# Kernel tuning notes

Measured on AMD Instinct MI355X. Metric: run time of the kernel, lower is better.

The kernel has to match this reference:

```python
import jax, jax.numpy as jnp
import numpy as np

N_USERS, N_ITEMS, N_ARTISTS, N_ALBUMS = 100000, 500000, 100000, 200000
D = 128
B, K = 4096, 64


def setup_inputs() -> dict:
    key = jax.random.key(0)
    ks = jax.random.split(key, 12)
    std = 1.0 / np.sqrt(D)
    pairs_u = jax.random.randint(ks[0], (B, 1), 0, N_USERS)
    pairs_i = jax.random.randint(ks[1], (B, 1), 0, N_ITEMS)
    return {
        "user_positive_items_pairs": jnp.concatenate([pairs_u, pairs_i], axis=1),
        "pos_artists": jax.random.randint(ks[2], (B,), 0, N_ARTISTS),
        "pos_albums": jax.random.randint(ks[3], (B,), 0, N_ALBUMS),
        "neg_samples": jax.random.randint(ks[4], (B, K), 0, N_ITEMS),
        "neg_artists": jax.random.randint(ks[5], (B, K), 0, N_ARTISTS),
        "neg_albums": jax.random.randint(ks[6], (B, K), 0, N_ALBUMS),
        "titles": jax.random.randint(ks[7], (B, 1), 0, 50000),
        "titles_len": jnp.ones((B,), dtype=jnp.int32),
        "Wu": jax.random.normal(ks[8], (N_USERS, D), dtype=jnp.float32) * std,
        "Wi": jax.random.normal(ks[9], (N_ITEMS, D), dtype=jnp.float32) * std,
        "Wart": jax.random.normal(ks[10], (N_ARTISTS, D), dtype=jnp.float32) * std,
        "Walb": jax.random.normal(ks[11], (N_ALBUMS, D), dtype=jnp.float32) * std,
    }


def reference(user_positive_items_pairs, pos_artists, pos_albums, neg_samples,
              neg_artists, neg_albums, titles, titles_len, Wu, Wi, Wart, Walb):
    # users: (B, D)
    users = Wu[user_positive_items_pairs[:, 0]]
    # positive combined item embedding: (B, D)
    pos_items = (Wi[user_positive_items_pairs[:, 1]] + Wart[pos_artists] + Walb[pos_albums]) / 3.0
    pos_distances = jnp.sum((users - pos_items) ** 2, axis=1)  # (B,)
    # negative combined item embeddings: (B, K, D)
    neg_items = (Wi[neg_samples] + Wart[neg_artists] + Walb[neg_albums]) / 3.0
    # squared distance to each negative: (B, K)
    distance_to_neg_items = jnp.sum((users[:, None, :] - neg_items) ** 2, axis=2)
    closest_negative_item_distances = jnp.min(distance_to_neg_items, axis=1)  # (B,)
    return pos_distances, distance_to_neg_items, closest_negative_item_distances
```

## Files before the change

kernel.cpp:

```cpp
#include <hip/hip_runtime.h>
#include <math.h>


__device__ __forceinline__ float halfwave_sum(float v) {
    #pragma unroll
    for (int off = 16; off; off >>= 1) v += __shfl_xor(v, off);
    return v;
}

__global__ __launch_bounds__(256) void cml_dist_kernel(
    const int* __restrict__ pairs,
    const int* __restrict__ pos_art,
    const int* __restrict__ pos_alb,
    const int* __restrict__ neg_samp,
    const int* __restrict__ neg_art,
    const int* __restrict__ neg_alb,
    const float4* __restrict__ Wu,
    const float4* __restrict__ Wi,
    const float4* __restrict__ Wart,
    const float4* __restrict__ Walb,
    float* __restrict__ out_pos,
    float* __restrict__ out_dist,
    float* __restrict__ out_min,
    int Kn)
{
    const int b    = blockIdx.x;
    const int tid  = threadIdx.x;
    const int lane = tid & 31;
    const int hw   = tid >> 5;

    __shared__ float s_dist[64];

    const int u_idx = pairs[2 * b];
    const float4 u = Wu[(size_t)u_idx * 32 + lane];

    const float inv3 = 1.0f / 3.0f;

    if (hw == 0) {
        const int ii = pairs[2 * b + 1];
        const int ia = pos_art[b];
        const int il = pos_alb[b];
        const float4 a = Wi  [(size_t)ii * 32 + lane];
        const float4 r = Wart[(size_t)ia * 32 + lane];
        const float4 l = Walb[(size_t)il * 32 + lane];
        const float dx = u.x - (a.x + r.x + l.x) * inv3;
        const float dy = u.y - (a.y + r.y + l.y) * inv3;
        const float dz = u.z - (a.z + r.z + l.z) * inv3;
        const float dw = u.w - (a.w + r.w + l.w) * inv3;
        float acc = dx * dx + dy * dy + dz * dz + dw * dw;
        acc = halfwave_sum(acc);
        if (lane == 0) out_pos[b] = acc;
    }

    for (int kk = hw; kk < Kn; kk += 8) {
        const int base = b * Kn + kk;
        const int ii = neg_samp[base];
        const int ia = neg_art [base];
        const int il = neg_alb [base];
        const float4 a = Wi  [(size_t)ii * 32 + lane];
        const float4 r = Wart[(size_t)ia * 32 + lane];
        const float4 l = Walb[(size_t)il * 32 + lane];
        const float dx = u.x - (a.x + r.x + l.x) * inv3;
        const float dy = u.y - (a.y + r.y + l.y) * inv3;
        const float dz = u.z - (a.z + r.z + l.z) * inv3;
        const float dw = u.w - (a.w + r.w + l.w) * inv3;
        float acc = dx * dx + dy * dy + dz * dz + dw * dw;
        acc = halfwave_sum(acc);
        if (lane == 0) {
            out_dist[base] = acc;
            s_dist[kk]     = acc;
        }
    }

    __syncthreads();

    if (tid < 64) {
        float v = (tid < Kn) ? s_dist[tid] : INFINITY;
        #pragma unroll
        for (int off = 32; off; off >>= 1) {
            const float o = __shfl_down(v, off, 64);
            v = fminf(v, o);
        }
        if (tid == 0) out_min[b] = v;
    }
}

extern "C" void kernel_launch(void* const* d_in, const int* in_sizes, int n_in,
                              void* d_out, int out_size, void* d_ws, size_t ws_size,
                              hipStream_t stream) {
    const int* pairs    = (const int*)d_in[0];
    const int* pos_art  = (const int*)d_in[1];
    const int* pos_alb  = (const int*)d_in[2];
    const int* neg_samp = (const int*)d_in[3];
    const int* neg_art  = (const int*)d_in[4];
    const int* neg_alb  = (const int*)d_in[5];
    const float4* Wu   = (const float4*)d_in[8];
    const float4* Wi   = (const float4*)d_in[9];
    const float4* Wart = (const float4*)d_in[10];
    const float4* Walb = (const float4*)d_in[11];

    const int Bn = in_sizes[1];
    const int Kn = in_sizes[3] / Bn;

    float* out      = (float*)d_out;
    float* out_pos  = out;
    float* out_dist = out + Bn;
    float* out_min  = out + Bn + (size_t)Bn * Kn;

    cml_dist_kernel<<<Bn, 256, 0, stream>>>(
        pairs, pos_art, pos_alb, neg_samp, neg_art, neg_alb,
        Wu, Wi, Wart, Walb, out_pos, out_dist, out_min, Kn);
}
```

Measured before the change: 445.8 us.

## Split into flat per-negative distance kernel and separate pos/min kernel

Replaces the one-block-per-batch-row kernel with a flat grid where each half-wave computes a single negative distance, so there is no per-row loop or block-wide barrier. A second small kernel computes the positive distance and the row minimum by reading back the stored negative distances. The aim is more memory-level parallelism and better load balance across the random-gather workload. In exchange, the user row is re-gathered once per negative, there is an extra launch plus an output re-read, and pos_min_kernel assumes K equals 64.

```diff
diff --git a/kernel.cpp b/kernel.cpp
--- a/kernel.cpp
+++ b/kernel.cpp
@@ -8,10 +8,8 @@
     return v;
 }
 
-__global__ __launch_bounds__(256) void cml_dist_kernel(
+__global__ __launch_bounds__(256) void neg_dist_kernel(
     const int* __restrict__ pairs,
-    const int* __restrict__ pos_art,
-    const int* __restrict__ pos_alb,
     const int* __restrict__ neg_samp,
     const int* __restrict__ neg_art,
     const int* __restrict__ neg_alb,
@@ -19,70 +17,70 @@
     const float4* __restrict__ Wi,
     const float4* __restrict__ Wart,
     const float4* __restrict__ Walb,
+    float* __restrict__ out_dist,
+    int total, int Kn)
+{
+    const int lane = threadIdx.x & 31;
+    const int g    = blockIdx.x * 8 + (threadIdx.x >> 5);
+    if (g >= total) return;
+    const int b = g / Kn;
+
+    const int ii = neg_samp[g];
+    const int ia = neg_art [g];
+    const int il = neg_alb [g];
+    const int ui = pairs[2 * b];
+
+    const float4 u = Wu  [(size_t)ui * 32 + lane];
+    const float4 a = Wi  [(size_t)ii * 32 + lane];
+    const float4 r = Wart[(size_t)ia * 32 + lane];
+    const float4 l = Walb[(size_t)il * 32 + lane];
+
+    const float inv3 = 1.0f / 3.0f;
+    const float dx = u.x - (a.x + r.x + l.x) * inv3;
+    const float dy = u.y - (a.y + r.y + l.y) * inv3;
+    const float dz = u.z - (a.z + r.z + l.z) * inv3;
+    const float dw = u.w - (a.w + r.w + l.w) * inv3;
+    float acc = dx * dx + dy * dy + dz * dz + dw * dw;
+    acc = halfwave_sum(acc);
+    if (lane == 0) out_dist[g] = acc;
+}
+
+__global__ __launch_bounds__(64) void pos_min_kernel(
+    const int* __restrict__ pairs,
+    const int* __restrict__ pos_art,
+    const int* __restrict__ pos_alb,
+    const float2* __restrict__ Wu,
+    const float2* __restrict__ Wi,
+    const float2* __restrict__ Wart,
+    const float2* __restrict__ Walb,
+    const float* __restrict__ out_dist,
     float* __restrict__ out_pos,
-    float* __restrict__ out_dist,
     float* __restrict__ out_min,
     int Kn)
 {
     const int b    = blockIdx.x;
-    const int tid  = threadIdx.x;
-    const int lane = tid & 31;
-    const int hw   = tid >> 5;
+    const int lane = threadIdx.x;
 
-    __shared__ float s_dist[64];
+    float m = out_dist[b * Kn + lane];
+    #pragma unroll
+    for (int off = 32; off; off >>= 1) m = fminf(m, __shfl_xor(m, off));
+    if (lane == 0) out_min[b] = m;
 
-    const int u_idx = pairs[2 * b];
-    const float4 u = Wu[(size_t)u_idx * 32 + lane];
-
+    const int ui = pairs[2 * b];
+    const int ii = pairs[2 * b + 1];
+    const int ia = pos_art[b];
+    const int il = pos_alb[b];
+    const float2 u = Wu  [(size_t)ui * 64 + lane];
+    const float2 a = Wi  [(size_t)ii * 64 + lane];
+    const float2 r = Wart[(size_t)ia * 64 + lane];
+    const float2 l = Walb[(size_t)il * 64 + lane];
     const float inv3 = 1.0f / 3.0f;
-
-    if (hw == 0) {
-        const int ii = pairs[2 * b + 1];
-        const int ia = pos_art[b];
-        const int il = pos_alb[b];
-        const float4 a = Wi  [(size_t)ii * 32 + lane];
-        const float4 r = Wart[(size_t)ia * 32 + lane];
-        const float4 l = Walb[(size_t)il * 32 + lane];
-        const float dx = u.x - (a.x + r.x + l.x) * inv3;
-        const float dy = u.y - (a.y + r.y + l.y) * inv3;
-        const float dz = u.z - (a.z + r.z + l.z) * inv3;
-        const float dw = u.w - (a.w + r.w + l.w) * inv3;
-        float acc = dx * dx + dy * dy + dz * dz + dw * dw;
-        acc = halfwave_sum(acc);
-        if (lane == 0) out_pos[b] = acc;
-    }
-
-    for (int kk = hw; kk < Kn; kk += 8) {
-        const int base = b * Kn + kk;
-        const int ii = neg_samp[base];
-        const int ia = neg_art [base];
-        const int il = neg_alb [base];
-        const float4 a = Wi  [(size_t)ii * 32 + lane];
-        const float4 r = Wart[(size_t)ia * 32 + lane];
-        const float4 l = Walb[(size_t)il * 32 + lane];
-        const float dx = u.x - (a.x + r.x + l.x) * inv3;
-        const float dy = u.y - (a.y + r.y + l.y) * inv3;
-        const float dz = u.z - (a.z + r.z + l.z) * inv3;
-        const float dw = u.w - (a.w + r.w + l.w) * inv3;
-        float acc = dx * dx + dy * dy + dz * dz + dw * dw;
-        acc = halfwave_sum(acc);
-        if (lane == 0) {
-            out_dist[base] = acc;
-            s_dist[kk]     = acc;
-        }
-    }
-
-    __syncthreads();
-
-    if (tid < 64) {
-        float v = (tid < Kn) ? s_dist[tid] : INFINITY;
-        #pragma unroll
-        for (int off = 32; off; off >>= 1) {
-            const float o = __shfl_down(v, off, 64);
-            v = fminf(v, o);
-        }
-        if (tid == 0) out_min[b] = v;
-    }
+    const float dx = u.x - (a.x + r.x + l.x) * inv3;
+    const float dy = u.y - (a.y + r.y + l.y) * inv3;
+    float acc = dx * dx + dy * dy;
+    #pragma unroll
+    for (int off = 32; off; off >>= 1) acc += __shfl_xor(acc, off);
+    if (lane == 0) out_pos[b] = acc;
 }
 
 extern "C" void kernel_launch(void* const* d_in, const int* in_sizes, int n_in,
@@ -94,20 +92,28 @@
     const int* neg_samp = (const int*)d_in[3];
     const int* neg_art  = (const int*)d_in[4];
     const int* neg_alb  = (const int*)d_in[5];
-    const float4* Wu   = (const float4*)d_in[8];
-    const float4* Wi   = (const float4*)d_in[9];
-    const float4* Wart = (const float4*)d_in[10];
-    const float4* Walb = (const float4*)d_in[11];
+    const float* Wu   = (const float*)d_in[8];
+    const float* Wi   = (const float*)d_in[9];
+    const float* Wart = (const float*)d_in[10];
+    const float* Walb = (const float*)d_in[11];
 
     const int Bn = in_sizes[1];
     const int Kn = in_sizes[3] / Bn;
+    const int total = Bn * Kn;
 
     float* out      = (float*)d_out;
     float* out_pos  = out;
     float* out_dist = out + Bn;
     float* out_min  = out + Bn + (size_t)Bn * Kn;
 
-    cml_dist_kernel<<<Bn, 256, 0, stream>>>(
-        pairs, pos_art, pos_alb, neg_samp, neg_art, neg_alb,
-        Wu, Wi, Wart, Walb, out_pos, out_dist, out_min, Kn);
+    const int blocks1 = (total + 7) / 8;
+    neg_dist_kernel<<<blocks1, 256, 0, stream>>>(
+        pairs, neg_samp, neg_art, neg_alb,
+        (const float4*)Wu, (const float4*)Wi, (const float4*)Wart, (const float4*)Walb,
+        out_dist, total, Kn);
+
+    pos_min_kernel<<<Bn, 64, 0, stream>>>(
+        pairs, pos_art, pos_alb,
+        (const float2*)Wu, (const float2*)Wi, (const float2*)Wart, (const float2*)Walb,
+        out_dist, out_pos, out_min, Kn);
 }
```

New measurement: 448.0 us. About the same (+0.5%).

## Batch negative gathers per half-wave with shuffled indices and nontemporal item loads

Applied to the files above, without the earlier changes.

Each half-wave now loads its 8 negative indices once, with one lane per index, and broadcasts them by shuffle. It issues 4 negatives' gathers at a time (12 float4 loads in flight) before computing, which raises memory-level parallelism. Item-table loads use nontemporal hints to avoid polluting cache, and the final min is reduced per half-wave in registers and then across 8 shared slots. The kernel now hardcodes K=64 (8 half-waves x 8 negatives) and silently breaks for other K.

```diff
diff --git a/kernel.cpp b/kernel.cpp
--- a/kernel.cpp
+++ b/kernel.cpp
@@ -1,6 +1,8 @@
 #include <hip/hip_runtime.h>
 #include <math.h>
 
+
+typedef float vf4 __attribute__((ext_vector_type(4)));
 
 __device__ __forceinline__ float halfwave_sum(float v) {
     #pragma unroll
@@ -8,17 +10,27 @@
     return v;
 }
 
-__global__ __launch_bounds__(256) void cml_dist_kernel(
+__device__ __forceinline__ float dist_sq(vf4 u, vf4 a, vf4 r, vf4 l) {
+    const float inv3 = 1.0f / 3.0f;
+    const float dx = u.x - (a.x + r.x + l.x) * inv3;
+    const float dy = u.y - (a.y + r.y + l.y) * inv3;
+    const float dz = u.z - (a.z + r.z + l.z) * inv3;
+    const float dw = u.w - (a.w + r.w + l.w) * inv3;
+    float acc = dx * dx + dy * dy + dz * dz + dw * dw;
+    return halfwave_sum(acc);
+}
+
+__global__ __launch_bounds__(256) void cml_fused_kernel(
     const int* __restrict__ pairs,
     const int* __restrict__ pos_art,
     const int* __restrict__ pos_alb,
     const int* __restrict__ neg_samp,
     const int* __restrict__ neg_art,
     const int* __restrict__ neg_alb,
-    const float4* __restrict__ Wu,
-    const float4* __restrict__ Wi,
-    const float4* __restrict__ Wart,
-    const float4* __restrict__ Walb,
+    const vf4* __restrict__ Wu,
+    const vf4* __restrict__ Wi,
+    const vf4* __restrict__ Wart,
+    const vf4* __restrict__ Walb,
     float* __restrict__ out_pos,
     float* __restrict__ out_dist,
     float* __restrict__ out_min,
@@ -29,59 +41,63 @@
     const int lane = tid & 31;
     const int hw   = tid >> 5;
 
-    __shared__ float s_dist[64];
+    __shared__ float s_min[8];
 
-    const int u_idx = pairs[2 * b];
-    const float4 u = Wu[(size_t)u_idx * 32 + lane];
-
-    const float inv3 = 1.0f / 3.0f;
+    const int ui = pairs[2 * b];
+    const vf4 u = Wu[(size_t)ui * 32 + lane];
 
     if (hw == 0) {
         const int ii = pairs[2 * b + 1];
         const int ia = pos_art[b];
         const int il = pos_alb[b];
-        const float4 a = Wi  [(size_t)ii * 32 + lane];
-        const float4 r = Wart[(size_t)ia * 32 + lane];
-        const float4 l = Walb[(size_t)il * 32 + lane];
-        const float dx = u.x - (a.x + r.x + l.x) * inv3;
-        const float dy = u.y - (a.y + r.y + l.y) * inv3;
-        const float dz = u.z - (a.z + r.z + l.z) * inv3;
-        const float dw = u.w - (a.w + r.w + l.w) * inv3;
-        float acc = dx * dx + dy * dy + dz * dz + dw * dw;
-        acc = halfwave_sum(acc);
-        if (lane == 0) out_pos[b] = acc;
+        const vf4 a = Wi  [(size_t)ii * 32 + lane];
+        const vf4 r = Wart[(size_t)ia * 32 + lane];
+        const vf4 l = Walb[(size_t)il * 32 + lane];
+        const float d = dist_sq(u, a, r, l);
+        if (lane == 0) out_pos[b] = d;
     }
 
-    for (int kk = hw; kk < Kn; kk += 8) {
-        const int base = b * Kn + kk;
-        const int ii = neg_samp[base];
-        const int ia = neg_art [base];
-        const int il = neg_alb [base];
-        const float4 a = Wi  [(size_t)ii * 32 + lane];
-        const float4 r = Wart[(size_t)ia * 32 + lane];
-        const float4 l = Walb[(size_t)il * 32 + lane];
-        const float dx = u.x - (a.x + r.x + l.x) * inv3;
-        const float dy = u.y - (a.y + r.y + l.y) * inv3;
-        const float dz = u.z - (a.z + r.z + l.z) * inv3;
-        const float dw = u.w - (a.w + r.w + l.w) * inv3;
-        float acc = dx * dx + dy * dy + dz * dz + dw * dw;
-        acc = halfwave_sum(acc);
-        if (lane == 0) {
-            out_dist[base] = acc;
-            s_dist[kk]     = acc;
-        }
+    const int kbase = b * Kn + hw * 8;
+    int v_samp = 0, v_art = 0, v_alb = 0;
+    if (lane < 8) {
+        v_samp = neg_samp[kbase + lane];
+        v_art  = neg_art [kbase + lane];
+        v_alb  = neg_alb [kbase + lane];
     }
 
+    float m = INFINITY;
+
+    #pragma unroll
+    for (int batch = 0; batch < 2; ++batch) {
+        vf4 A[4], R[4], L[4];
+        #pragma unroll
+        for (int j = 0; j < 4; ++j) {
+            const int jj = batch * 4 + j;
+            const int ii = __shfl(v_samp, jj, 32);
+            const int ia = __shfl(v_art,  jj, 32);
+            const int il = __shfl(v_alb,  jj, 32);
+            A[j] = __builtin_nontemporal_load(&Wi[(size_t)ii * 32 + lane]);
+            R[j] = Wart[(size_t)ia * 32 + lane];
+            L[j] = Walb[(size_t)il * 32 + lane];
+        }
+        float myd = 0.0f;
+        #pragma unroll
+        for (int j = 0; j < 4; ++j) {
+            const float d = dist_sq(u, A[j], R[j], L[j]);
+            m = fminf(m, d);
+            if (lane == j) myd = d;
+        }
+        if (lane < 4) out_dist[kbase + batch * 4 + lane] = myd;
+    }
+
+    if (lane == 0) s_min[hw] = m;
     __syncthreads();
 
-    if (tid < 64) {
-        float v = (tid < Kn) ? s_dist[tid] : INFINITY;
+    if (tid == 0) {
+        float mm = s_min[0];
         #pragma unroll
-        for (int off = 32; off; off >>= 1) {
-            const float o = __shfl_down(v, off, 64);
-            v = fminf(v, o);
-        }
-        if (tid == 0) out_min[b] = v;
+        for (int i = 1; i < 8; ++i) mm = fminf(mm, s_min[i]);
+        out_min[b] = mm;
     }
 }
 
@@ -94,10 +110,10 @@
     const int* neg_samp = (const int*)d_in[3];
     const int* neg_art  = (const int*)d_in[4];
     const int* neg_alb  = (const int*)d_in[5];
-    const float4* Wu   = (const float4*)d_in[8];
-    const float4* Wi   = (const float4*)d_in[9];
-    const float4* Wart = (const float4*)d_in[10];
-    const float4* Walb = (const float4*)d_in[11];
+    const vf4* Wu   = (const vf4*)d_in[8];
+    const vf4* Wi   = (const vf4*)d_in[9];
+    const vf4* Wart = (const vf4*)d_in[10];
+    const vf4* Walb = (const vf4*)d_in[11];
 
     const int Bn = in_sizes[1];
     const int Kn = in_sizes[3] / Bn;
@@ -107,7 +123,7 @@
     float* out_dist = out + Bn;
     float* out_min  = out + Bn + (size_t)Bn * Kn;
 
-    cml_dist_kernel<<<Bn, 256, 0, stream>>>(
+    cml_fused_kernel<<<Bn, 256, 0, stream>>>(
         pairs, pos_art, pos_alb, neg_samp, neg_art, neg_alb,
         Wu, Wi, Wart, Walb, out_pos, out_dist, out_min, Kn);
 }
```

New measurement: 438.3 us. About the same (-1.7%).
